# Kernel optimization log

Measured on AMD Instinct MI355X. Metric: run time of the kernel, lower is better.

The kernel has to match this reference:

```python
import jax, jax.numpy as jnp
import numpy as np

T, B, E, H, L, V = 35, 128, 200, 512, 2, 10000


def setup_inputs() -> dict:
    key = jax.random.key(0)
    ks = jax.random.split(key, 8)
    s = 0.05  # weight init scale
    return {
        "inputs": jax.random.randint(ks[0], (T, B), 0, V),
        "hidden": jnp.zeros((L, B, H), jnp.float32),
        "emb": jax.random.normal(ks[1], (V, E), jnp.float32) * s,
        "Wx0": jax.random.normal(ks[2], (3, H, E), jnp.float32) * s,
        "Wx": jax.random.normal(ks[3], (L - 1, 3, H, H), jnp.float32) * s,
        "Wh": jax.random.normal(ks[4], (L, 3, H, H), jnp.float32) * s,
        "bh": jax.random.normal(ks[5], (L, 3, H), jnp.float32) * s,
        "Wout": jax.random.normal(ks[6], (V, H), jnp.float32) * s,
        "bout": jnp.zeros((V,), jnp.float32),
    }


def reference(inputs, hidden, emb, Wx0, Wx, Wh, bh, Wout, bout):
    # inputs: [T,B] int; hidden: [L,B,H]
    x = emb[inputs]  # [T,B,E]
    num_layers = hidden.shape[0]

    def step(h_prev, x_t):
        data = x_t  # dropout is identity (keep_prob=1.0)
        new_h = []
        for j in range(num_layers):
            Wxj = Wx0 if j == 0 else Wx[j - 1]
            gx = jnp.einsum('bi,ghi->gbh', data, Wxj)  # [3,B,H], no bias on x-side
            hp = h_prev[j]
            reset = jax.nn.sigmoid(gx[0] + hp @ Wh[j, 0].T + bh[j, 0])
            forget = jax.nn.sigmoid(gx[1] + hp @ Wh[j, 1].T + bh[j, 1])
            tild = jnp.tanh(gx[2] + (reset * hp) @ Wh[j, 2].T + bh[j, 2])
            hn = (1.0 - forget) * hp + forget * tild
            new_h.append(hn)
            data = hn  # dropout identity
        logit = data @ Wout.T + bout  # [B,V]
        return jnp.stack(new_h), logit

    h_final, logits = jax.lax.scan(step, hidden, x)
    return logits, h_final
```

## Files before the change

kernel.cpp:

```cpp
#include <hip/hip_runtime.h>
#include <hip/hip_bf16.h>

#define T_ 35
#define B_ 128
#define E_ 200
#define H_ 512
#define L_ 2
#define V_ 10000
#define BH_ (B_ * H_)
#define KPAD 224
#define NCL 4
#define CLW 48
#define NWG (NCL * CLW)

typedef __attribute__((ext_vector_type(8))) short bf16x8;
typedef __attribute__((ext_vector_type(4))) float f32x4;

__device__ __forceinline__ unsigned short f2bf(float f) {
    union { float f; unsigned u; } c; c.f = f;
    unsigned r = c.u + 0x7FFF + ((c.u >> 16) & 1);
    return (unsigned short)(r >> 16);
}
__device__ __forceinline__ float bf2f(unsigned short u) {
    union { unsigned u; float f; } c; c.u = ((unsigned)u) << 16; return c.f;
}

__device__ __forceinline__ bf16x8 cvt8(const float* src) {
    float4 w0 = *(const float4*)src;
    float4 w1 = *(const float4*)(src + 4);
    bf16x8 v;
    v[0] = (short)f2bf(w0.x); v[1] = (short)f2bf(w0.y);
    v[2] = (short)f2bf(w0.z); v[3] = (short)f2bf(w0.w);
    v[4] = (short)f2bf(w1.x); v[5] = (short)f2bf(w1.y);
    v[6] = (short)f2bf(w1.z); v[7] = (short)f2bf(w1.w);
    return v;
}

__device__ __forceinline__ void store_pair_bf16(unsigned short* buf, int idx,
                                                float v, int lane) {
    float vn = __shfl_xor(v, 1);
    if ((lane & 1) == 0) {
        unsigned p = (unsigned)f2bf(v) | ((unsigned)f2bf(vn) << 16);
        __hip_atomic_store((unsigned*)(buf + idx), p,
                           __ATOMIC_RELAXED, __HIP_MEMORY_SCOPE_AGENT);
    }
}

__global__ void prep_all(const float* __restrict__ emb, const float* __restrict__ Wx0,
                         const float* __restrict__ hidden, const float* __restrict__ Wout,
                         unsigned short* embB, unsigned short* wx0cat,
                         unsigned short* WoutB,
                         unsigned short* h0bt, unsigned short* h1bfx, int* flags) {
    int job = blockIdx.y;
    int stride = gridDim.x * blockDim.x;
    int i0 = blockIdx.x * blockDim.x + threadIdx.x;
    if (job == 0) {
        for (int i = i0; i < V_ * KPAD; i += stride) {
            int v = i / KPAD, k = i - v * KPAD;
            embB[i] = (k < E_) ? f2bf(emb[v * E_ + k]) : (unsigned short)0;
        }
    } else if (job == 1) {
        for (int i = i0; i < 1536 * KPAD; i += stride) {
            int n = i / KPAD, k = i - n * KPAD;
            wx0cat[i] = (k < E_) ? f2bf(Wx0[n * E_ + k]) : (unsigned short)0;
        }
    } else if (job == 2) {
        for (int i = i0; i < 2 * BH_; i += stride) {
            if (i < BH_) h0bt[i] = f2bf(hidden[i]);
            else         h1bfx[i - BH_] = f2bf(hidden[i]);
        }
        for (int i = i0; i < NWG * 32; i += stride) flags[i] = 0;
    } else {
        for (int i = i0; i < V_ * H_; i += stride) WoutB[i] = f2bf(Wout[i]);
    }
}

__global__ __launch_bounds__(256) void xside_gemm(
    const int* __restrict__ inputs, const unsigned short* __restrict__ embB,
    const unsigned short* __restrict__ wx0cat, float* __restrict__ gx0) {
    int m0 = blockIdx.x * 128, n0 = blockIdx.y * 128;
    int wave = threadIdx.x >> 6, lane = threadIdx.x & 63;
    int wr = wave >> 1, wc = wave & 1;
    int am = m0 + wr * 64, bn = n0 + wc * 64;
    int lr = lane & 15, lk = (lane >> 4) * 8;

    f32x4 acc[4][4] = {};
    int id[4];
    #pragma unroll
    for (int i = 0; i < 4; ++i) id[i] = inputs[am + i * 16 + lr];

    for (int k0 = 0; k0 < KPAD; k0 += 32) {
        bf16x8 a[4], b[4];
        #pragma unroll
        for (int i = 0; i < 4; ++i)
            a[i] = *(const bf16x8*)(embB + (size_t)id[i] * KPAD + k0 + lk);
        #pragma unroll
        for (int j = 0; j < 4; ++j)
            b[j] = *(const bf16x8*)(wx0cat + (size_t)(bn + j * 16 + lr) * KPAD + k0 + lk);
        #pragma unroll
        for (int i = 0; i < 4; ++i)
            #pragma unroll
            for (int j = 0; j < 4; ++j)
                acc[i][j] = __builtin_amdgcn_mfma_f32_16x16x32_bf16(a[i], b[j], acc[i][j], 0, 0, 0);
    }
    int crow0 = (lane >> 4) * 4, ccol = lane & 15;
    #pragma unroll
    for (int i = 0; i < 4; ++i) {
        #pragma unroll
        for (int r = 0; r < 4; ++r) {
            int row = am + i * 16 + crow0 + r;
            int t = row >> 7, b = row & 127;
            #pragma unroll
            for (int j = 0; j < 4; ++j) {
                int col = bn + j * 16 + ccol;
                int g = col >> 9, h = col & 511;
                gx0[((size_t)(t * 3 + g) * 128 + b) * 512 + h] = acc[i][j][r];
            }
        }
    }
}

__device__ __forceinline__ void bar_l0(int* flb, int wgl, int gen) {
    __syncthreads();
    if (threadIdx.x == 0)
        __hip_atomic_store(flb + wgl * 32, gen,
                           __ATOMIC_RELAXED, __HIP_MEMORY_SCOPE_AGENT);
    if (threadIdx.x < 16) {
        while (__hip_atomic_load(flb + threadIdx.x * 32, __ATOMIC_RELAXED,
                                 __HIP_MEMORY_SCOPE_AGENT) < gen)
            __builtin_amdgcn_s_sleep(1);
    }
    __syncthreads();
}

__device__ __forceinline__ void bar_l1(int* flb, int wid, int gen, int l0need) {
    __syncthreads();
    if (threadIdx.x == 0)
        __hip_atomic_store(flb + (16 + wid) * 32, gen,
                           __ATOMIC_RELAXED, __HIP_MEMORY_SCOPE_AGENT);
    if (threadIdx.x < 32) {
        while (__hip_atomic_load(flb + (16 + threadIdx.x) * 32, __ATOMIC_RELAXED,
                                 __HIP_MEMORY_SCOPE_AGENT) < gen)
            __builtin_amdgcn_s_sleep(1);
    } else if (threadIdx.x < 48) {
        while (__hip_atomic_load(flb + (threadIdx.x - 32) * 32, __ATOMIC_RELAXED,
                                 __HIP_MEMORY_SCOPE_AGENT) < l0need)
            __builtin_amdgcn_s_sleep(1);
    }
    __syncthreads();
}

__global__ __launch_bounds__(512) void scan_kernel(
    const float* __restrict__ gx0,
    const float* __restrict__ Wx, const float* __restrict__ Wh,
    const float* __restrict__ bh, const float* __restrict__ hidden,
    unsigned short* h0bt, unsigned short* rh0t, unsigned short* rh1t,
    unsigned short* h1bfx, int* flags, float* hfinal_out) {
    __shared__ unsigned short wlds[96 * 512];

    const int tid = threadIdx.x;
    const int bx = blockIdx.x;
    const int cl = bx & 3;
    const int wgl = bx >> 2;
    const int lane = tid & 63;
    const int wave = tid >> 6;
    const int lr = lane & 15;
    const int hi = lane >> 4;
    const int lk8 = hi * 8;
    const int ccol = lane & 15;
    const int crow0 = hi * 4;
    const int R0 = cl * 32;

    const bool isL0 = (wgl < 16);
    const int wid = wgl - 16;
    int* flb = flags + cl * CLW * 32;

    if (isL0) {
        for (int i = tid; i < 96 * 64; i += 512) {
            int lc = i >> 6, kg = i & 63;
            int g = lc >> 5, h = (wgl << 5) + (lc & 31);
            const float* src = Wh + (size_t)(g * 512 + h) * 512 + kg * 8;
            *(bf16x8*)(wlds + lc * 512 + (kg ^ (lc & 7)) * 8) = cvt8(src);
        }
    } else {
        for (int i = tid; i < 48 * 128; i += 512) {
            int lc = i >> 7, kg = i & 127;
            int g = lc >> 4, h = (wid << 4) + (lc & 15);
            const float* src = (kg < 64)
                ? Wx + (size_t)(g * 512 + h) * 512 + kg * 8
                : Wh + (size_t)(3 * 512 * 512) + (size_t)(g * 512 + h) * 512 + (kg - 64) * 8;
            *(bf16x8*)(wlds + lc * 1024 + (kg ^ (lc & 7)) * 8) = cvt8(src);
        }
    }

    const int mt0 = wave >> 2, nt0 = wave & 3;
    const int mt1 = (wave >> 1) & 1, nt1 = wave & 1;
    float h0reg[4], freg0[4], bias_p1_0 = 0.f, bias_p2_0 = 0.f;
    float h1reg[4], freg1[4], bias_p1_1 = 0.f, bias_p2_1 = 0.f;
    bf16x8 a0keep[16];

    if (isL0) {
        const int base = wgl << 5;
        int g = nt0 >> 1;
        int hp1 = base + (nt0 & 1) * 16 + ccol;
        bias_p1_0 = bh[g * 512 + hp1];
        if (nt0 >= 2) {
            int hc = base + (nt0 - 2) * 16 + ccol;
            int rowg = R0 + mt0 * 16;
            #pragma unroll
            for (int r = 0; r < 4; ++r)
                h0reg[r] = hidden[(size_t)(rowg + crow0 + r) * 512 + hc];
            bias_p2_0 = bh[1024 + hc];
        }
    } else {
        const int base = wid << 4;
        int hc = base + ccol;
        if (wave < 4) {
            bias_p1_1 = bh[1536 + nt1 * 512 + hc];
            if (nt1 == 1) {
                int rowg = R0 + mt1 * 16;
                #pragma unroll
                for (int r = 0; r < 4; ++r)
                    h1reg[r] = hidden[(size_t)BH_ + (size_t)(rowg + crow0 + r) * 512 + hc];
                bias_p2_1 = bh[2560 + hc];
            }
        }
    }
    __syncthreads();

    if (isL0) {
        for (int s = 0; s < 2 * T_; ++s) {
            bar_l0(flb, wgl, s);
            int t = s >> 1;
            if ((s & 1) == 0) {
                const int base = wgl << 5;
                const int rowg = R0 + mt0 * 16;
                const unsigned short* hprev = h0bt + (size_t)t * BH_;
                unsigned short* rh0 = rh0t + (size_t)t * BH_;
                bf16x8 a[16];
                #pragma unroll
                for (int ks = 0; ks < 16; ++ks)
                    a[ks] = *(const bf16x8*)(hprev + (size_t)(rowg + lr) * 512 + ks * 32 + lk8);
                int g = nt0 >> 1;
                int h = base + (nt0 & 1) * 16 + ccol;
                float gxv[4];
                {
                    const float* gx = gx0 + (size_t)(t * 3 + g) * BH_ + h;
                    #pragma unroll
                    for (int r = 0; r < 4; ++r)
                        gxv[r] = gx[(rowg + crow0 + r) * 512];
                }
                f32x4 accA = {0.f, 0.f, 0.f, 0.f}, accB = {0.f, 0.f, 0.f, 0.f};
                #pragma unroll
                for (int ks = 0; ks < 16; ks += 2) {
                    int c = nt0 * 16 + lr;
                    int kgA = 4 * ks + hi, kgB = 4 * (ks + 1) + hi;
                    bf16x8 bA = *(const bf16x8*)(wlds + c * 512 + (kgA ^ (c & 7)) * 8);
                    bf16x8 bB = *(const bf16x8*)(wlds + c * 512 + (kgB ^ (c & 7)) * 8);
                    accA = __builtin_amdgcn_mfma_f32_16x16x32_bf16(a[ks], bA, accA, 0, 0, 0);
                    accB = __builtin_amdgcn_mfma_f32_16x16x32_bf16(a[ks + 1], bB, accB, 0, 0, 0);
                }
                #pragma unroll
                for (int r = 0; r < 4; ++r) {
                    int b = rowg + crow0 + r;
                    float v = accA[r] + accB[r] + gxv[r] + bias_p1_0;
                    float sg = 1.f / (1.f + __expf(-v));
                    if (nt0 < 2) {
                        float h0p = bf2f(hprev[(size_t)b * 512 + h]);
                        store_pair_bf16(rh0, b * 512 + h, sg * h0p, lane);
                    } else {
                        freg0[r] = sg;
                    }
                }
            } else if (nt0 >= 2) {
                const int base = wgl << 5;
                const int ntp = nt0 - 2;
                const int rowg = R0 + mt0 * 16;
                const unsigned short* rh0 = rh0t + (size_t)t * BH_;
                unsigned short* h0nx = h0bt + (size_t)(t + 1) * BH_;
                bf16x8 a[16];
                #pragma unroll
                for (int ks = 0; ks < 16; ++ks)
                    a[ks] = *(const bf16x8*)(rh0 + (size_t)(rowg + lr) * 512 + ks * 32 + lk8);
                int h = base + ntp * 16 + ccol;
                float gxv[4];
                {
                    const float* gx = gx0 + (size_t)(t * 3 + 2) * BH_ + h;
                    #pragma unroll
                    for (int r = 0; r < 4; ++r)
                        gxv[r] = gx[(rowg + crow0 + r) * 512];
                }
                f32x4 accA = {0.f, 0.f, 0.f, 0.f}, accB = {0.f, 0.f, 0.f, 0.f};
                #pragma unroll
                for (int ks = 0; ks < 16; ks += 2) {
                    int c = 64 + ntp * 16 + lr;
                    int kgA = 4 * ks + hi, kgB = 4 * (ks + 1) + hi;
                    bf16x8 bA = *(const bf16x8*)(wlds + c * 512 + (kgA ^ (c & 7)) * 8);
                    bf16x8 bB = *(const bf16x8*)(wlds + c * 512 + (kgB ^ (c & 7)) * 8);
                    accA = __builtin_amdgcn_mfma_f32_16x16x32_bf16(a[ks], bA, accA, 0, 0, 0);
                    accB = __builtin_amdgcn_mfma_f32_16x16x32_bf16(a[ks + 1], bB, accB, 0, 0, 0);
                }
                #pragma unroll
                for (int r = 0; r < 4; ++r) {
                    int b = rowg + crow0 + r;
                    float v = accA[r] + accB[r] + gxv[r] + bias_p2_0;
                    float tld = tanhf(v);
                    float hn = h0reg[r] + freg0[r] * (tld - h0reg[r]);
                    h0reg[r] = hn;
                    store_pair_bf16(h0nx, b * 512 + h, hn, lane);
                }
            }
        }
        __syncthreads();
        if (tid == 0)
            __hip_atomic_store(flb + wgl * 32, 2 * T_,
                               __ATOMIC_RELAXED, __HIP_MEMORY_SCOPE_AGENT);
        if (nt0 >= 2) {
            const int base = wgl << 5;
            int hc = base + (nt0 - 2) * 16 + ccol;
            int rowg = R0 + mt0 * 16;
            #pragma unroll
            for (int r = 0; r < 4; ++r)
                hfinal_out[(size_t)(rowg + crow0 + r) * 512 + hc] = h0reg[r];
        }
    } else {
        for (int s = 0; s < 2 * T_; ++s) {
            int tc = s >> 1;
            int l0need = ((s & 1) == 0) ? (2 * tc + 2) : 0;
            bar_l1(flb, wid, s, l0need);
            if ((s & 1) == 0) {
                if (wave < 4) {
                    const int base = wid << 4;
                    const int rowg = R0 + mt1 * 16;
                    const unsigned short* h0cur = h0bt + (size_t)(tc + 1) * BH_;
                    const unsigned short* h1prev = h1bfx + (size_t)tc * BH_;
                    unsigned short* rh1 = rh1t + (size_t)tc * BH_;
                    bf16x8 a1[16];
                    #pragma unroll
                    for (int ks = 0; ks < 16; ++ks) {
                        a0keep[ks] = *(const bf16x8*)(h0cur + (size_t)(rowg + lr) * 512 + ks * 32 + lk8);
                        a1[ks] = *(const bf16x8*)(h1prev + (size_t)(rowg + lr) * 512 + ks * 32 + lk8);
                    }
                    f32x4 accA = {0.f, 0.f, 0.f, 0.f}, accB = {0.f, 0.f, 0.f, 0.f};
                    #pragma unroll
                    for (int ks = 0; ks < 16; ++ks) {
                        int kg = 4 * ks + hi;
                        int c = nt1 * 16 + lr;
                        bf16x8 b = *(const bf16x8*)(wlds + c * 1024 + (kg ^ (c & 7)) * 8);
                        accA = __builtin_amdgcn_mfma_f32_16x16x32_bf16(a0keep[ks], b, accA, 0, 0, 0);
                    }
                    #pragma unroll
                    for (int ks = 0; ks < 16; ++ks) {
                        int kg = 64 + 4 * ks + hi;
                        int c = nt1 * 16 + lr;
                        bf16x8 b = *(const bf16x8*)(wlds + c * 1024 + (kg ^ (c & 7)) * 8);
                        accB = __builtin_amdgcn_mfma_f32_16x16x32_bf16(a1[ks], b, accB, 0, 0, 0);
                    }
                    int h = base + ccol;
                    #pragma unroll
                    for (int r = 0; r < 4; ++r) {
                        int b = rowg + crow0 + r;
                        float v = accA[r] + accB[r] + bias_p1_1;
                        float sg = 1.f / (1.f + __expf(-v));
                        if (nt1 == 0) {
                            float h1p = bf2f(h1prev[(size_t)b * 512 + h]);
                            store_pair_bf16(rh1, b * 512 + h, sg * h1p, lane);
                        } else {
                            freg1[r] = sg;
                        }
                    }
                }
            } else {
                if (wave < 4 && nt1 == 1) {
                    const int base = wid << 4;
                    const int rowg = R0 + mt1 * 16;
                    const unsigned short* rh1 = rh1t + (size_t)tc * BH_;
                    unsigned short* h1nx = h1bfx + (size_t)(tc + 1) * BH_;
                    bf16x8 a1[16];
                    #pragma unroll
                    for (int ks = 0; ks < 16; ++ks)
                        a1[ks] = *(const bf16x8*)(rh1 + (size_t)(rowg + lr) * 512 + ks * 32 + lk8);
                    f32x4 accA = {0.f, 0.f, 0.f, 0.f}, accB = {0.f, 0.f, 0.f, 0.f};
                    #pragma unroll
                    for (int ks = 0; ks < 16; ++ks) {
                        int kg = 4 * ks + hi;
                        int c = 32 + lr;
                        bf16x8 b = *(const bf16x8*)(wlds + c * 1024 + (kg ^ (c & 7)) * 8);
                        accA = __builtin_amdgcn_mfma_f32_16x16x32_bf16(a0keep[ks], b, accA, 0, 0, 0);
                    }
                    #pragma unroll
                    for (int ks = 0; ks < 16; ++ks) {
                        int kg = 64 + 4 * ks + hi;
                        int c = 32 + lr;
                        bf16x8 b = *(const bf16x8*)(wlds + c * 1024 + (kg ^ (c & 7)) * 8);
                        accB = __builtin_amdgcn_mfma_f32_16x16x32_bf16(a1[ks], b, accB, 0, 0, 0);
                    }
                    int h = base + ccol;
                    #pragma unroll
                    for (int r = 0; r < 4; ++r) {
                        int b = rowg + crow0 + r;
                        float v = accA[r] + accB[r] + bias_p2_1;
                        float tld = tanhf(v);
                        float hn = h1reg[r] + freg1[r] * (tld - h1reg[r]);
                        h1reg[r] = hn;
                        store_pair_bf16(h1nx, b * 512 + h, hn, lane);
                    }
                }
            }
        }
        if (wave < 4 && nt1 == 1) {
            const int base = wid << 4;
            int rowg = R0 + mt1 * 16;
            #pragma unroll
            for (int r = 0; r < 4; ++r)
                hfinal_out[(size_t)BH_ + (size_t)(rowg + crow0 + r) * 512 + base + ccol] = h1reg[r];
        }
    }
}

#define MT_ (T_ * B_ / 128)
#define NT_ ((V_ + 127) / 128)
__global__ __launch_bounds__(256) void logits_gemm(
    const unsigned short* __restrict__ A, const unsigned short* __restrict__ Bw,
    const float* __restrict__ bout, float* __restrict__ C) {
    const int nwg = MT_ * NT_;
    const int q = nwg / 8, rr = nwg % 8;
    int bid = blockIdx.x;
    int xcd = bid % 8, idx = bid / 8;
    int wgid = (xcd < rr ? xcd * (q + 1) : rr * (q + 1) + (xcd - rr) * q) + idx;
    int n0 = (wgid / MT_) * 128;
    int m0 = (wgid % MT_) * 128;

    int wave = threadIdx.x >> 6, lane = threadIdx.x & 63;
    int wr = wave >> 1, wc = wave & 1;
    int am = m0 + wr * 64, bn = n0 + wc * 64;
    int lr = lane & 15, lk = (lane >> 4) * 8;

    f32x4 acc[4][4] = {};
    bf16x8 a[4], b[4], an[4], bnx[4];
    #pragma unroll
    for (int i = 0; i < 4; ++i)
        a[i] = *(const bf16x8*)(A + (size_t)(am + i * 16 + lr) * H_ + lk);
    #pragma unroll
    for (int j = 0; j < 4; ++j) {
        int colc = bn + j * 16 + lr; if (colc >= V_) colc = V_ - 1;
        b[j] = *(const bf16x8*)(Bw + (size_t)colc * H_ + lk);
    }
    for (int k0 = 0; k0 < H_; k0 += 32) {
        if (k0 + 32 < H_) {
            #pragma unroll
            for (int i = 0; i < 4; ++i)
                an[i] = *(const bf16x8*)(A + (size_t)(am + i * 16 + lr) * H_ + k0 + 32 + lk);
            #pragma unroll
            for (int j = 0; j < 4; ++j) {
                int colc = bn + j * 16 + lr; if (colc >= V_) colc = V_ - 1;
                bnx[j] = *(const bf16x8*)(Bw + (size_t)colc * H_ + k0 + 32 + lk);
            }
        }
        #pragma unroll
        for (int i = 0; i < 4; ++i)
            #pragma unroll
            for (int j = 0; j < 4; ++j)
                acc[i][j] = __builtin_amdgcn_mfma_f32_16x16x32_bf16(a[i], b[j], acc[i][j], 0, 0, 0);
        #pragma unroll
        for (int i = 0; i < 4; ++i) { a[i] = an[i]; b[i] = bnx[i]; }
    }
    int crow0 = (lane >> 4) * 4, ccol = lane & 15;
    #pragma unroll
    for (int j = 0; j < 4; ++j) {
        int col = bn + j * 16 + ccol;
        if (col >= V_) continue;
        float bv = bout[col];
        #pragma unroll
        for (int i = 0; i < 4; ++i) {
            #pragma unroll
            for (int r = 0; r < 4; ++r) {
                int row = am + i * 16 + crow0 + r;
                __builtin_nontemporal_store(acc[i][j][r] + bv, &C[(size_t)row * V_ + col]);
            }
        }
    }
}

extern "C" void kernel_launch(void* const* d_in, const int* in_sizes, int n_in,
                              void* d_out, int out_size, void* d_ws, size_t ws_size,
                              hipStream_t stream) {
    const int*   inputs = (const int*)  d_in[0];
    const float* hidden = (const float*)d_in[1];
    const float* emb    = (const float*)d_in[2];
    const float* Wx0    = (const float*)d_in[3];
    const float* Wx     = (const float*)d_in[4];
    const float* Wh     = (const float*)d_in[5];
    const float* bh     = (const float*)d_in[6];
    const float* Wout   = (const float*)d_in[7];
    const float* bout   = (const float*)d_in[8];
    float* out = (float*)d_out;
    (void)in_sizes; (void)n_in; (void)out_size; (void)ws_size;

    char* ws = (char*)d_ws;
    size_t off = 0;
    auto alloc = [&](size_t bytes) -> void* {
        void* p = ws + off;
        off += (bytes + 255) & ~(size_t)255;
        return p;
    };
    unsigned short* embB   = (unsigned short*)alloc((size_t)V_ * KPAD * 2);
    unsigned short* wx0cat = (unsigned short*)alloc((size_t)1536 * KPAD * 2);
    unsigned short* WoutB  = (unsigned short*)alloc((size_t)V_ * H_ * 2);
    unsigned short* h1bfx  = (unsigned short*)alloc((size_t)(T_ + 1) * BH_ * 2);
    int* flags = (int*)alloc(NWG * 32 * 4);

    float* gx0 = out;
    unsigned short* scr = (unsigned short*)(out + (size_t)T_ * 3 * BH_);
    unsigned short* h0bt = scr;
    unsigned short* rh0t = scr + (size_t)(T_ + 1) * BH_;
    unsigned short* rh1t = scr + (size_t)(2 * T_ + 1) * BH_;

    prep_all<<<dim3(1024, 4), dim3(256), 0, stream>>>(
        emb, Wx0, hidden, Wout, embB, wx0cat, WoutB, h0bt, h1bfx, flags);
    xside_gemm<<<dim3(T_, 12), dim3(256), 0, stream>>>(inputs, embB, wx0cat, gx0);
    scan_kernel<<<dim3(NWG), dim3(512), 0, stream>>>(
        gx0, Wx, Wh, bh, hidden,
        h0bt, rh0t, rh1t, h1bfx, flags,
        out + (size_t)T_ * B_ * V_);
    logits_gemm<<<dim3(MT_ * NT_), dim3(256), 0, stream>>>(
        h1bfx + BH_, WoutB, bout, out);
}
```

Measured before the change: 602.6 us.

## Pin GRU scan workgroups to XCCs and use XCC-local barriers

```diff
diff --git a/kernel.cpp b/kernel.cpp
--- a/kernel.cpp
+++ b/kernel.cpp
@@ -10,8 +10,7 @@
 #define BH_ (B_ * H_)
 #define KPAD 224
 #define NCL 4
-#define CLW 48
-#define NWG (NCL * CLW)
+#define GRID_WG 512
 
 typedef __attribute__((ext_vector_type(8))) short bf16x8;
 typedef __attribute__((ext_vector_type(4))) float f32x4;
@@ -24,7 +23,6 @@
 __device__ __forceinline__ float bf2f(unsigned short u) {
     union { unsigned u; float f; } c; c.u = ((unsigned)u) << 16; return c.f;
 }
-
 __device__ __forceinline__ bf16x8 cvt8(const float* src) {
     float4 w0 = *(const float4*)src;
     float4 w1 = *(const float4*)(src + 4);
@@ -35,7 +33,12 @@
     v[6] = (short)f2bf(w1.z); v[7] = (short)f2bf(w1.w);
     return v;
 }
-
+__device__ __forceinline__ bf16x8 vld8(const unsigned short* p) {
+    return *(const volatile bf16x8*)p;
+}
+__device__ __forceinline__ unsigned short vld2(const unsigned short* p) {
+    return *(const volatile unsigned short*)p;
+}
 __device__ __forceinline__ void store_pair_bf16(unsigned short* buf, int idx,
                                                 float v, int lane) {
     float vn = __shfl_xor(v, 1);
@@ -46,11 +49,14 @@
     }
 }
 
+#define CTRL_INTS 6528
+
 __global__ void prep_all(const float* __restrict__ emb, const float* __restrict__ Wx0,
                          const float* __restrict__ hidden, const float* __restrict__ Wout,
                          unsigned short* embB, unsigned short* wx0cat,
                          unsigned short* WoutB,
-                         unsigned short* h0bt, unsigned short* h1bfx, int* flags) {
+                         unsigned short* h0loc, unsigned short* h0mall,
+                         unsigned short* h1bfx, int* ctrl) {
     int job = blockIdx.y;
     int stride = gridDim.x * blockDim.x;
     int i0 = blockIdx.x * blockDim.x + threadIdx.x;
@@ -66,10 +72,14 @@
         }
     } else if (job == 2) {
         for (int i = i0; i < 2 * BH_; i += stride) {
-            if (i < BH_) h0bt[i] = f2bf(hidden[i]);
-            else         h1bfx[i - BH_] = f2bf(hidden[i]);
-        }
-        for (int i = i0; i < NWG * 32; i += stride) flags[i] = 0;
+            if (i < BH_) {
+                unsigned short b = f2bf(hidden[i]);
+                h0loc[i] = b; h0mall[i] = b;
+            } else {
+                h1bfx[i - BH_] = f2bf(hidden[i]);
+            }
+        }
+        for (int i = i0; i < CTRL_INTS; i += stride) ctrl[i] = 0;
     } else {
         for (int i = i0; i < V_ * H_; i += stride) WoutB[i] = f2bf(Wout[i]);
     }
@@ -120,31 +130,11 @@
     }
 }
 
-__device__ __forceinline__ void bar_l0(int* flb, int wgl, int gen) {
+__device__ __forceinline__ void bar_loc(int* fl, int my, int first, int n, int gen) {
     __syncthreads();
-    if (threadIdx.x == 0)
-        __hip_atomic_store(flb + wgl * 32, gen,
-                           __ATOMIC_RELAXED, __HIP_MEMORY_SCOPE_AGENT);
-    if (threadIdx.x < 16) {
-        while (__hip_atomic_load(flb + threadIdx.x * 32, __ATOMIC_RELAXED,
-                                 __HIP_MEMORY_SCOPE_AGENT) < gen)
-            __builtin_amdgcn_s_sleep(1);
-    }
-    __syncthreads();
-}
-
-__device__ __forceinline__ void bar_l1(int* flb, int wid, int gen, int l0need) {
-    __syncthreads();
-    if (threadIdx.x == 0)
-        __hip_atomic_store(flb + (16 + wid) * 32, gen,
-                           __ATOMIC_RELAXED, __HIP_MEMORY_SCOPE_AGENT);
-    if (threadIdx.x < 32) {
-        while (__hip_atomic_load(flb + (16 + threadIdx.x) * 32, __ATOMIC_RELAXED,
-                                 __HIP_MEMORY_SCOPE_AGENT) < gen)
-            __builtin_amdgcn_s_sleep(1);
-    } else if (threadIdx.x < 48) {
-        while (__hip_atomic_load(flb + (threadIdx.x - 32) * 32, __ATOMIC_RELAXED,
-                                 __HIP_MEMORY_SCOPE_AGENT) < l0need)
+    if (threadIdx.x == 0) *(volatile int*)(fl + my * 32) = gen;
+    if (threadIdx.x < n) {
+        while (*(volatile int*)(fl + (first + threadIdx.x) * 32) < gen)
             __builtin_amdgcn_s_sleep(1);
     }
     __syncthreads();
@@ -154,14 +144,27 @@
     const float* __restrict__ gx0,
     const float* __restrict__ Wx, const float* __restrict__ Wh,
     const float* __restrict__ bh, const float* __restrict__ hidden,
-    unsigned short* h0bt, unsigned short* rh0t, unsigned short* rh1t,
-    unsigned short* h1bfx, int* flags, float* hfinal_out) {
-    __shared__ unsigned short wlds[96 * 512];
+    unsigned short* h0loc, unsigned short* h0mall,
+    unsigned short* rh0loc, unsigned short* rh1loc,
+    unsigned short* h1bfx, int* ctrl, float* hfinal_out) {
+    __shared__ unsigned short wlds[48 * 1024];
+    __shared__ int slot_sh;
 
     const int tid = threadIdx.x;
-    const int bx = blockIdx.x;
-    const int cl = bx & 3;
-    const int wgl = bx >> 2;
+    int xcc;
+    asm volatile("s_getreg_b32 %0, hwreg(HW_REG_XCC_ID)" : "=s"(xcc));
+    xcc &= 7;
+    if (tid == 0)
+        slot_sh = __hip_atomic_fetch_add(ctrl + 6272 + xcc * 32, 1,
+                                         __ATOMIC_RELAXED, __HIP_MEMORY_SCOPE_AGENT);
+    __syncthreads();
+    const int slot = slot_sh;
+    const bool isL0 = (xcc < 4);
+    const int cl = xcc & 3;
+    if (isL0 ? (slot >= 16) : (slot >= 32)) return;
+    const int wgl = slot;
+    const int wid = slot;
+
     const int lane = tid & 63;
     const int wave = tid >> 6;
     const int lr = lane & 15;
@@ -171,9 +174,8 @@
     const int crow0 = hi * 4;
     const int R0 = cl * 32;
 
-    const bool isL0 = (wgl < 16);
-    const int wid = wgl - 16;
-    int* flb = flags + cl * CLW * 32;
+    int* flags = ctrl + cl * 48 * 32;
+    int* mallgen = ctrl + 6144 + cl * 32;
 
     if (isL0) {
         for (int i = tid; i < 96 * 64; i += 512) {
@@ -230,17 +232,16 @@
 
     if (isL0) {
         for (int s = 0; s < 2 * T_; ++s) {
-            bar_l0(flb, wgl, s);
             int t = s >> 1;
             if ((s & 1) == 0) {
                 const int base = wgl << 5;
                 const int rowg = R0 + mt0 * 16;
-                const unsigned short* hprev = h0bt + (size_t)t * BH_;
-                unsigned short* rh0 = rh0t + (size_t)t * BH_;
+                const unsigned short* hprev = h0loc + (size_t)t * BH_;
+                unsigned short* rh0 = rh0loc + (size_t)t * BH_;
                 bf16x8 a[16];
                 #pragma unroll
                 for (int ks = 0; ks < 16; ++ks)
-                    a[ks] = *(const bf16x8*)(hprev + (size_t)(rowg + lr) * 512 + ks * 32 + lk8);
+                    a[ks] = vld8(hprev + (size_t)(rowg + lr) * 512 + ks * 32 + lk8);
                 int g = nt0 >> 1;
                 int h = base + (nt0 & 1) * 16 + ccol;
                 float gxv[4];
@@ -266,8 +267,8 @@
                     float v = accA[r] + accB[r] + gxv[r] + bias_p1_0;
                     float sg = 1.f / (1.f + __expf(-v));
                     if (nt0 < 2) {
-                        float h0p = bf2f(hprev[(size_t)b * 512 + h]);
-                        store_pair_bf16(rh0, b * 512 + h, sg * h0p, lane);
+                        float h0p = bf2f(vld2(hprev + (size_t)b * 512 + h));
+                        rh0[(size_t)b * 512 + h] = f2bf(sg * h0p);
                     } else {
                         freg0[r] = sg;
                     }
@@ -276,12 +277,13 @@
                 const int base = wgl << 5;
                 const int ntp = nt0 - 2;
                 const int rowg = R0 + mt0 * 16;
-                const unsigned short* rh0 = rh0t + (size_t)t * BH_;
-                unsigned short* h0nx = h0bt + (size_t)(t + 1) * BH_;
+                const unsigned short* rh0 = rh0loc + (size_t)t * BH_;
+                unsigned short* h0nxl = h0loc + (size_t)(t + 1) * BH_;
+                unsigned short* h0nxm = h0mall + (size_t)(t + 1) * BH_;
                 bf16x8 a[16];
                 #pragma unroll
                 for (int ks = 0; ks < 16; ++ks)
-                    a[ks] = *(const bf16x8*)(rh0 + (size_t)(rowg + lr) * 512 + ks * 32 + lk8);
+                    a[ks] = vld8(rh0 + (size_t)(rowg + lr) * 512 + ks * 32 + lk8);
                 int h = base + ntp * 16 + ccol;
                 float gxv[4];
                 {
@@ -307,14 +309,15 @@
                     float tld = tanhf(v);
                     float hn = h0reg[r] + freg0[r] * (tld - h0reg[r]);
                     h0reg[r] = hn;
-                    store_pair_bf16(h0nx, b * 512 + h, hn, lane);
-                }
-            }
-        }
-        __syncthreads();
-        if (tid == 0)
-            __hip_atomic_store(flb + wgl * 32, 2 * T_,
-                               __ATOMIC_RELAXED, __HIP_MEMORY_SCOPE_AGENT);
+                    h0nxl[(size_t)b * 512 + h] = f2bf(hn);
+                    store_pair_bf16(h0nxm, b * 512 + h, hn, lane);
+                }
+            }
+            bar_loc(flags, wgl, 0, 16, s + 1);
+            if (wgl == 0 && tid == 0)
+                __hip_atomic_store(mallgen, s + 1, __ATOMIC_RELAXED,
+                                   __HIP_MEMORY_SCOPE_AGENT);
+        }
         if (nt0 >= 2) {
             const int base = wgl << 5;
             int hc = base + (nt0 - 2) * 16 + ccol;
@@ -326,20 +329,24 @@
     } else {
         for (int s = 0; s < 2 * T_; ++s) {
             int tc = s >> 1;
-            int l0need = ((s & 1) == 0) ? (2 * tc + 2) : 0;
-            bar_l1(flb, wid, s, l0need);
             if ((s & 1) == 0) {
+                if (tid == 0) {
+                    while (__hip_atomic_load(mallgen, __ATOMIC_RELAXED,
+                                             __HIP_MEMORY_SCOPE_AGENT) < 2 * tc + 2)
+                        __builtin_amdgcn_s_sleep(1);
+                }
+                __syncthreads();
                 if (wave < 4) {
                     const int base = wid << 4;
                     const int rowg = R0 + mt1 * 16;
-                    const unsigned short* h0cur = h0bt + (size_t)(tc + 1) * BH_;
+                    const unsigned short* h0cur = h0mall + (size_t)(tc + 1) * BH_;
                     const unsigned short* h1prev = h1bfx + (size_t)tc * BH_;
-                    unsigned short* rh1 = rh1t + (size_t)tc * BH_;
+                    unsigned short* rh1 = rh1loc + (size_t)tc * BH_;
                     bf16x8 a1[16];
                     #pragma unroll
                     for (int ks = 0; ks < 16; ++ks) {
                         a0keep[ks] = *(const bf16x8*)(h0cur + (size_t)(rowg + lr) * 512 + ks * 32 + lk8);
-                        a1[ks] = *(const bf16x8*)(h1prev + (size_t)(rowg + lr) * 512 + ks * 32 + lk8);
+                        a1[ks] = vld8(h1prev + (size_t)(rowg + lr) * 512 + ks * 32 + lk8);
                     }
                     f32x4 accA = {0.f, 0.f, 0.f, 0.f}, accB = {0.f, 0.f, 0.f, 0.f};
                     #pragma unroll
@@ -363,8 +370,8 @@
                         float v = accA[r] + accB[r] + bias_p1_1;
                         float sg = 1.f / (1.f + __expf(-v));
                         if (nt1 == 0) {
-                            float h1p = bf2f(h1prev[(size_t)b * 512 + h]);
-                            store_pair_bf16(rh1, b * 512 + h, sg * h1p, lane);
+                            float h1p = bf2f(vld2(h1prev + (size_t)b * 512 + h));
+                            rh1[(size_t)b * 512 + h] = f2bf(sg * h1p);
                         } else {
                             freg1[r] = sg;
                         }
@@ -374,12 +381,12 @@
                 if (wave < 4 && nt1 == 1) {
                     const int base = wid << 4;
                     const int rowg = R0 + mt1 * 16;
-                    const unsigned short* rh1 = rh1t + (size_t)tc * BH_;
+                    const unsigned short* rh1 = rh1loc + (size_t)tc * BH_;
                     unsigned short* h1nx = h1bfx + (size_t)(tc + 1) * BH_;
                     bf16x8 a1[16];
                     #pragma unroll
                     for (int ks = 0; ks < 16; ++ks)
-                        a1[ks] = *(const bf16x8*)(rh1 + (size_t)(rowg + lr) * 512 + ks * 32 + lk8);
+                        a1[ks] = vld8(rh1 + (size_t)(rowg + lr) * 512 + ks * 32 + lk8);
                     f32x4 accA = {0.f, 0.f, 0.f, 0.f}, accB = {0.f, 0.f, 0.f, 0.f};
                     #pragma unroll
                     for (int ks = 0; ks < 16; ++ks) {
@@ -403,10 +410,11 @@
                         float tld = tanhf(v);
                         float hn = h1reg[r] + freg1[r] * (tld - h1reg[r]);
                         h1reg[r] = hn;
-                        store_pair_bf16(h1nx, b * 512 + h, hn, lane);
-                    }
-                }
-            }
+                        h1nx[(size_t)b * 512 + h] = f2bf(hn);
+                    }
+                }
+            }
+            bar_loc(flags, 16 + wid, 16, 32, s + 1);
         }
         if (wave < 4 && nt1 == 1) {
             const int base = wid << 4;
@@ -508,20 +516,21 @@
     unsigned short* wx0cat = (unsigned short*)alloc((size_t)1536 * KPAD * 2);
     unsigned short* WoutB  = (unsigned short*)alloc((size_t)V_ * H_ * 2);
     unsigned short* h1bfx  = (unsigned short*)alloc((size_t)(T_ + 1) * BH_ * 2);
-    int* flags = (int*)alloc(NWG * 32 * 4);
+    int* ctrl = (int*)alloc((size_t)CTRL_INTS * 4);
 
     float* gx0 = out;
     unsigned short* scr = (unsigned short*)(out + (size_t)T_ * 3 * BH_);
-    unsigned short* h0bt = scr;
-    unsigned short* rh0t = scr + (size_t)(T_ + 1) * BH_;
-    unsigned short* rh1t = scr + (size_t)(2 * T_ + 1) * BH_;
+    unsigned short* h0loc  = scr;
+    unsigned short* h0mall = scr + (size_t)(T_ + 1) * BH_;
+    unsigned short* rh0loc = scr + (size_t)(2 * T_ + 2) * BH_;
+    unsigned short* rh1loc = scr + (size_t)(3 * T_ + 2) * BH_;
 
     prep_all<<<dim3(1024, 4), dim3(256), 0, stream>>>(
-        emb, Wx0, hidden, Wout, embB, wx0cat, WoutB, h0bt, h1bfx, flags);
+        emb, Wx0, hidden, Wout, embB, wx0cat, WoutB, h0loc, h0mall, h1bfx, ctrl);
     xside_gemm<<<dim3(T_, 12), dim3(256), 0, stream>>>(inputs, embB, wx0cat, gx0);
-    scan_kernel<<<dim3(NWG), dim3(512), 0, stream>>>(
+    scan_kernel<<<dim3(GRID_WG), dim3(512), 0, stream>>>(
         gx0, Wx, Wh, bh, hidden,
-        h0bt, rh0t, rh1t, h1bfx, flags,
+        h0loc, h0mall, rh0loc, rh1loc, h1bfx, ctrl,
         out + (size_t)T_ * B_ * V_);
     logits_gemm<<<dim3(MT_ * NT_), dim3(256), 0, stream>>>(
         h1bfx + BH_, WoutB, bout, out);
```

Measured after the change: 737.6 us. +22.4%, slower.
